# Optimization experiments

Measured on AMD Instinct MI355X. Metric: run time of the kernel, lower is better.

## Reference

```python
import jax, jax.numpy as jnp
import numpy as np
from jax import lax

# ---- config constants (mirror init_kwargs) ----
PC_MIN_X, PC_MIN_Y, PC_MIN_Z = 0.0, -40.0, -3.0
PC_MAX_X, PC_MAX_Y, PC_MAX_Z = 70.4, 40.0, 1.0
VX, VY = 0.05, 0.05
NUM_KEYPOINTS = 2048
RADII = (0.4, 0.8)
NSAMPLE = (16, 16)
EPS = 1e-5


def setup_inputs() -> dict:
    key = jax.random.key(0)
    ks = jax.random.split(key, 16)
    B, N = 2, 32768
    u = jax.random.uniform(ks[0], (B, N, 4), dtype=jnp.float32)
    x = u[..., 0] * (PC_MAX_X - PC_MIN_X) + PC_MIN_X
    y = u[..., 1] * (PC_MAX_Y - PC_MIN_Y) + PC_MIN_Y
    z = u[..., 2] * (PC_MAX_Z - PC_MIN_Z) + PC_MIN_Z
    points = jnp.stack([x, y, z, u[..., 3]], axis=-1)  # (B,N,4): xyz + intensity
    spatial_features = jax.random.normal(ks[1], (B, 256, 200, 176), dtype=jnp.float32)
    p = lambda k, s: jax.random.normal(k, s, dtype=jnp.float32) * 0.1
    return dict(
        points=points, spatial_features=spatial_features,
        w0_0=p(ks[2], (4, 16)), g0_0=jnp.ones(16), b0_0=jnp.zeros(16),
        w0_1=p(ks[3], (16, 16)), g0_1=jnp.ones(16), b0_1=jnp.zeros(16),
        w1_0=p(ks[4], (4, 16)), g1_0=jnp.ones(16), b1_0=jnp.zeros(16),
        w1_1=p(ks[5], (16, 16)), g1_1=jnp.ones(16), b1_1=jnp.zeros(16),
        wf=p(ks[6], (288, 128)), gf=jnp.ones(128), bf=jnp.zeros(128),
        bev_stride=8,
    )


def _bn(x, g, b, axes):
    m = jnp.mean(x, axis=axes, keepdims=True)
    v = jnp.var(x, axis=axes, keepdims=True)
    return (x - m) * lax.rsqrt(v + EPS) * g + b


def _fps(xyz, K):
    # farthest point sampling, pointnet2 semantics (start at index 0)
    B, N, _ = xyz.shape
    def step(carry, _):
        dists, last = carry
        p = jax.vmap(lambda a, i: a[i])(xyz, last)           # (B,3)
        d = jnp.sum((xyz - p[:, None, :]) ** 2, axis=-1)     # (B,N)
        dists = jnp.minimum(dists, d)
        nxt = jnp.argmax(dists, axis=-1).astype(jnp.int32)
        return (dists, nxt), nxt
    init = (jnp.full((B, N), 1e10, xyz.dtype), jnp.zeros((B,), jnp.int32))
    _, rest = lax.scan(step, init, None, length=K - 1)       # (K-1,B)
    return jnp.concatenate([jnp.zeros((B, 1), jnp.int32), rest.T], axis=1)  # (B,K)


def _ball_group_pool(pts, kp, dist2, radius, ns, layers):
    # pts: (B,N,4) xyz+feat, kp: (B,K,3), dist2: (B,K,N) (stop-grad)
    B, N = pts.shape[0], pts.shape[1]
    valid = dist2 < radius * radius
    score = jnp.where(valid, -jnp.arange(N, dtype=jnp.float32), -jnp.inf)
    vals, idx = lax.top_k(score, ns)                          # first ns in-radius indices
    ok = jnp.isfinite(vals)                                   # (B,K,ns)
    idx = jnp.where(ok, idx, idx[..., :1])                    # duplicate first valid
    empty = ~ok[..., 0]                                       # (B,K) no neighbor at all
    grouped = jax.vmap(lambda p, i: p[i])(pts, idx)           # (B,K,ns,4)
    rel = grouped[..., :3] - kp[:, :, None, :]
    h = jnp.concatenate([rel, grouped[..., 3:]], axis=-1)     # (B,K,ns,4)
    h = jnp.where(empty[..., None, None], 0.0, h)
    for w, g, b in layers:
        h = jax.nn.relu(_bn(h @ w, g, b, axes=(0, 1, 2)))
    pooled = jnp.max(h, axis=2)                               # (B,K,C)
    return jnp.where(empty[..., None], 0.0, pooled)


def _bev_interp(kp, bev, stride):
    # kp: (B,K,3), bev: (B,C,H,W); torch bilinear_interpolate semantics
    B, C, H, W = bev.shape
    xi = (kp[..., 0] - PC_MIN_X) / VX / stride                # (B,K)
    yi = (kp[..., 1] - PC_MIN_Y) / VY / stride
    x0 = jnp.clip(jnp.floor(xi).astype(jnp.int32), 0, W - 1)
    x1 = jnp.clip(jnp.floor(xi).astype(jnp.int32) + 1, 0, W - 1)
    y0 = jnp.clip(jnp.floor(yi).astype(jnp.int32), 0, H - 1)
    y1 = jnp.clip(jnp.floor(yi).astype(jnp.int32) + 1, 0, H - 1)
    gat = jax.vmap(lambda f, yy, xx: f[:, yy, xx].T)          # (K,C) per batch
    Ia, Ib = gat(bev, y0, x0), gat(bev, y1, x0)
    Ic, Id = gat(bev, y0, x1), gat(bev, y1, x1)
    x0f, x1f = x0.astype(jnp.float32), x1.astype(jnp.float32)
    y0f, y1f = y0.astype(jnp.float32), y1.astype(jnp.float32)
    wa = ((x1f - xi) * (y1f - yi))[..., None]
    wb = ((x1f - xi) * (yi - y0f))[..., None]
    wc = ((xi - x0f) * (y1f - yi))[..., None]
    wd = ((xi - x0f) * (yi - y0f))[..., None]
    return Ia * wa + Ib * wb + Ic * wc + Id * wd              # (B,K,C)


def reference(points, spatial_features, w0_0, g0_0, b0_0, w0_1, g0_1, b0_1,
              w1_0, g1_0, b1_0, w1_1, g1_1, b1_1, wf, gf, bf, bev_stride):
    xyz = points[..., :3]                                     # (B,N,3)
    idx = _fps(xyz, NUM_KEYPOINTS)                            # (B,K)
    kp = jax.vmap(lambda p, i: p[i])(xyz, idx)                # keypoints (B,K,3)

    # BEV bilinear interpolation
    bev_feats = _bev_interp(kp, spatial_features, bev_stride) # (B,K,256)

    # raw-points multi-scale ball-query aggregation
    dist2 = lax.stop_gradient(
        jnp.sum((kp[:, :, None, :] - xyz[:, None, :, :]) ** 2, axis=-1))  # (B,K,N)
    p0 = _ball_group_pool(points, kp, dist2, RADII[0], NSAMPLE[0],
                          [(w0_0, g0_0, b0_0), (w0_1, g0_1, b0_1)])
    p1 = _ball_group_pool(points, kp, dist2, RADII[1], NSAMPLE[1],
                          [(w1_0, g1_0, b1_0), (w1_1, g1_1, b1_1)])

    feat = jnp.concatenate([bev_feats, p0, p1], axis=-1)      # (B,K,288)
    M = feat.shape[0] * feat.shape[1]
    feat = feat.reshape(M, -1)
    h = feat @ wf                                             # Linear no bias
    h = _bn(h, gf, bf, axes=(0,))                             # BatchNorm1d (train mode)
    return jax.nn.relu(h)                                     # (M,128)
```

## Files before the change

kernel.cpp:

```cpp
#include <hip/hip_runtime.h>
#include <hip/hip_bf16.h>
#include <limits.h>
#include <cstddef>

#define B_SZ    2
#define N_PTS   32768
#define N_KP    2048
#define N_CHUNK 512
#define H_BEV   200
#define W_BEV   176
#define C_BEV   256
#define FEAT_DIM 288
#define C_OUT   128
#define M_ROWS  4096

__device__ __forceinline__ float sqd(float ax, float ay, float az,
                                     float bx, float by, float bz) {
  float dx = ax - bx, dy = ay - by, dz = az - bz;
  return __fadd_rn(__fadd_rn(dx * dx, dy * dy), dz * dz);
}

__device__ __forceinline__ unsigned part1by1(unsigned n) {
  n &= 0xFFFF;
  n = (n | (n << 8)) & 0x00FF00FF;
  n = (n | (n << 4)) & 0x0F0F0F0F;
  n = (n | (n << 2)) & 0x33333333;
  n = (n | (n << 1)) & 0x55555555;
  return n;
}

#define DPP_MOV(v, CTRL, RMASK) \
  ((unsigned)__builtin_amdgcn_update_dpp((int)(v), (int)(v), (CTRL), (RMASK), 0xf, false))

__device__ __forceinline__ unsigned wave_umax_bcast(unsigned v) {
  unsigned t;
  t = DPP_MOV(v, 0x111, 0xf); v = v > t ? v : t;
  t = DPP_MOV(v, 0x112, 0xf); v = v > t ? v : t;
  t = DPP_MOV(v, 0x114, 0xf); v = v > t ? v : t;
  t = DPP_MOV(v, 0x118, 0xf); v = v > t ? v : t;
  t = DPP_MOV(v, 0x142, 0xa); v = v > t ? v : t;
  t = DPP_MOV(v, 0x143, 0xc); v = v > t ? v : t;
  return (unsigned)__builtin_amdgcn_readlane((int)v, 63);
}
__device__ __forceinline__ unsigned wave_umin_bcast(unsigned v) {
  unsigned t;
  t = DPP_MOV(v, 0x111, 0xf); v = v < t ? v : t;
  t = DPP_MOV(v, 0x112, 0xf); v = v < t ? v : t;
  t = DPP_MOV(v, 0x114, 0xf); v = v < t ? v : t;
  t = DPP_MOV(v, 0x118, 0xf); v = v < t ? v : t;
  t = DPP_MOV(v, 0x142, 0xa); v = v < t ? v : t;
  t = DPP_MOV(v, 0x143, 0xc); v = v < t ? v : t;
  return (unsigned)__builtin_amdgcn_readlane((int)v, 63);
}

#define R64_STEP(hi, lo, CTRL, RMASK)                                         \
  {                                                                           \
    unsigned hm_ = DPP_MOV(hi, CTRL, RMASK);                                  \
    unsigned lm_ = DPP_MOV(lo, CTRL, RMASK);                                  \
    bool gt_ = (hm_ > (hi)) || (hm_ == (hi) && lm_ > (lo));                   \
    hi = gt_ ? hm_ : (hi); lo = gt_ ? lm_ : (lo);                             \
  }

#define R64_ALL(hi, lo)                                                       \
  R64_STEP(hi, lo, 0x111, 0xf)                                                \
  R64_STEP(hi, lo, 0x112, 0xf)                                                \
  R64_STEP(hi, lo, 0x114, 0xf)                                                \
  R64_STEP(hi, lo, 0x118, 0xf)                                                \
  R64_STEP(hi, lo, 0x142, 0xa)                                                \
  R64_STEP(hi, lo, 0x143, 0xc)

__global__ void cell_count(const float4* __restrict__ pts,
                           int* __restrict__ codes, int* __restrict__ counts) {
  const int b = blockIdx.x, tid = threadIdx.x;
  __shared__ int cnt[4096];
  for (int k = tid; k < 4096; k += 1024) cnt[k] = 0;
  __syncthreads();
  for (int j = 0; j < 32; ++j) {
    int i = j * 1024 + tid;
    float4 v = pts[(size_t)b * N_PTS + i];
    int cx = min(63, max(0, (int)(v.x * (64.0f / 70.4f))));
    int cy = min(63, max(0, (int)((v.y + 40.0f) * 0.8f)));
    int code = (int)(part1by1((unsigned)cx) | (part1by1((unsigned)cy) << 1));
    codes[(size_t)b * N_PTS + i] = code;
    atomicAdd(&cnt[code], 1);
  }
  __syncthreads();
  for (int k = tid; k < 4096; k += 1024) counts[b * 4096 + k] = cnt[k];
}

__global__ void cell_scan(const int* __restrict__ counts, int* __restrict__ offs) {
  const int b = blockIdx.x, lane = threadIdx.x;
  const int* cnt = counts + b * 4096;
  int* off = offs + b * 4096;
  int s = 0;
  for (int k = 0; k < 64; ++k) s += cnt[lane * 64 + k];
  int incl = s;
#pragma unroll
  for (int o = 1; o < 64; o <<= 1) {
    int t = __shfl_up(incl, o);
    if (lane >= o) incl += t;
  }
  int run = incl - s;
  for (int k = 0; k < 64; ++k) {
    int id = lane * 64 + k;
    int t = cnt[id];
    off[id] = run;
    run += t;
  }
}

__global__ void scatter_pts(const float4* __restrict__ pts,
                            const int* __restrict__ codes,
                            int* __restrict__ offs,
                            float4* __restrict__ spts, int* __restrict__ sorig) {
  const int b = blockIdx.x, tid = threadIdx.x;
  for (int j = 0; j < 32; ++j) {
    int i = j * 1024 + tid;
    int code = codes[(size_t)b * N_PTS + i];
    int pos = atomicAdd(&offs[b * 4096 + code], 1);
    spts[(size_t)b * N_PTS + pos] = pts[(size_t)b * N_PTS + i];
    sorig[(size_t)b * N_PTS + pos] = i;
  }
}

__global__ void chunk_bbox(const float4* __restrict__ spts, float* __restrict__ bbox) {
  const int wid = threadIdx.x >> 6, lane = threadIdx.x & 63;
  const int chunk = blockIdx.x * 4 + wid;
  const int b = chunk >> 9, c = chunk & (N_CHUNK - 1);
  float4 v = spts[(size_t)b * N_PTS + c * 64 + lane];
  float lx = v.x, ly = v.y, lz = v.z, hx = v.x, hy = v.y, hz = v.z;
#pragma unroll
  for (int o = 32; o >= 1; o >>= 1) {
    lx = fminf(lx, __shfl_xor(lx, o)); hx = fmaxf(hx, __shfl_xor(hx, o));
    ly = fminf(ly, __shfl_xor(ly, o)); hy = fmaxf(hy, __shfl_xor(hy, o));
    lz = fminf(lz, __shfl_xor(lz, o)); hz = fmaxf(hz, __shfl_xor(hz, o));
  }
  if (lane == 0) {
    float* bp = bbox + (size_t)chunk * 6;
    bp[0] = lx; bp[1] = ly; bp[2] = lz; bp[3] = hx; bp[4] = hy; bp[5] = hz;
  }
}

__global__ void fps_pruned(const float4* __restrict__ pts,
                           const float4* __restrict__ spts,
                           const int* __restrict__ sorig,
                           const float* __restrict__ bbox,
                           float4* __restrict__ kp_xyz) {
  const int b = blockIdx.x;
  const int tid = threadIdx.x;
  const int wid = tid >> 6, lane = tid & 63;
  const float4* p4o = pts + (size_t)b * N_PTS;
  const float4* sp4 = spts + (size_t)b * N_PTS;
  const int* sog = sorig + (size_t)b * N_PTS;
  const unsigned long long below = (lane == 0) ? 0ull : ((~0ull) >> (64 - lane));

  __shared__ float d_lds[N_PTS];
  __shared__ float keyd[N_CHUNK];
  __shared__ int keyo[N_CHUNK];
  __shared__ float keyx[N_CHUNK];
  __shared__ float keyy[N_CHUNK];
  __shared__ float keyz[N_CHUNK];
  __shared__ int dirty_s[2][N_CHUNK];
  __shared__ int ndirty_s[2];

  for (int i = tid; i < N_PTS; i += 1024) d_lds[i] = 1e10f;
  if (tid < N_CHUNK) keyd[tid] = 1e10f;
  if (tid < 2) ndirty_s[tid] = 0;
  float bx0 = 0.f, by0 = 0.f, bz0 = 0.f, bx1 = 0.f, by1 = 0.f, bz1 = 0.f;
  if (tid < N_CHUNK) {
    const float* bp = bbox + (size_t)b * N_CHUNK * 6 + (size_t)tid * 6;
    bx0 = bp[0]; by0 = bp[1]; bz0 = bp[2]; bx1 = bp[3]; by1 = bp[4]; bz1 = bp[5];
  }
  float4 p0 = p4o[0];
  float sx = p0.x, sy = p0.y, sz = p0.z;
  if (tid == 0) kp_xyz[b * N_KP] = make_float4(sx, sy, sz, 0.f);
  __syncthreads();

#define PROC_CHUNK(cc, pp, og, dp)                                            \
  {                                                                           \
    float ss = sqd((pp).x, (pp).y, (pp).z, sx, sy, sz);                       \
    float nd = fminf((dp), ss);                                               \
    d_lds[((cc) << 6) + lane] = nd;                                           \
    unsigned nb = __float_as_uint(nd);          \
    unsigned mb = wave_umax_bcast(nb);                                        \
    unsigned cnd = (nb == mb) ? (unsigned)(og) : 0xFFFFFFFFu;                 \
    cnd = wave_umin_bcast(cnd);                                               \
    if ((unsigned)(og) == cnd) {                                              \
      keyd[cc] = __uint_as_float(mb); keyo[cc] = (int)cnd;                    \
      keyx[cc] = (pp).x; keyy[cc] = (pp).y; keyz[cc] = (pp).z;                \
    }                                                                         \
  }

  for (int it = 1; it < N_KP; ++it) {
    const int s = it & 1;
    bool dirty = false;
    if (tid < N_CHUNK) {
      float dxm = fmaxf(fmaxf(bx0 - sx, sx - bx1), 0.f);
      float dym = fmaxf(fmaxf(by0 - sy, sy - by1), 0.f);
      float dzm = fmaxf(fmaxf(bz0 - sz, sz - bz1), 0.f);
      float lb = (dxm * dxm + dym * dym) + dzm * dzm;
      dirty = lb * 0.99999f < keyd[tid];
    }
    unsigned long long m = __ballot(dirty);
    if (tid < N_CHUNK) {
      int cw = (int)__popcll(m);
      int base = 0;
      if (lane == 0 && cw) base = atomicAdd(&ndirty_s[s], cw);
      base = __builtin_amdgcn_readfirstlane(base);
      if (dirty) dirty_s[s][base + (int)__popcll(m & below)] = tid;
    }
    if (tid == 1023) ndirty_s[s ^ 1] = 0;
    __syncthreads();
    const int K = ndirty_s[s];
    {
      int cA = (wid < K) ? dirty_s[s][wid] : -1;
      int cB = ((wid + 16) < K) ? dirty_s[s][wid + 16] : -1;
      if (cA >= 0) {
        int iA = (cA << 6) + lane;
        float4 pA = sp4[iA];
        int ogA = sog[iA];
        float dpA = d_lds[iA];
        if (cB >= 0) {
          int iB = (cB << 6) + lane;
          float4 pB = sp4[iB];
          int ogB = sog[iB];
          float dpB = d_lds[iB];
          PROC_CHUNK(cA, pA, ogA, dpA);
          PROC_CHUNK(cB, pB, ogB, dpB);
        } else {
          PROC_CHUNK(cA, pA, ogA, dpA);
        }
        for (int r = 2; r * 16 < K; ++r) {
          int ci = r * 16 + wid;
          if (ci < K) {
            int c = dirty_s[s][ci];
            int i2 = (c << 6) + lane;
            float4 p = sp4[i2];
            int og2 = sog[i2];
            float dp2 = d_lds[i2];
            PROC_CHUNK(c, p, og2, dp2);
          }
        }
      }
    }
    __syncthreads();
    {
      unsigned hi = __float_as_uint(keyd[lane]);
      unsigned lo = 0xFFFFFFFFu - (unsigned)keyo[lane];
      unsigned ch = (unsigned)lane;
#pragma unroll
      for (int j = 1; j < 8; ++j) {
        int c = j * 64 + lane;
        unsigned h2 = __float_as_uint(keyd[c]);
        unsigned l2 = 0xFFFFFFFFu - (unsigned)keyo[c];
        bool gt = (h2 > hi) || (h2 == hi && l2 > lo);
        hi = gt ? h2 : hi; lo = gt ? l2 : lo; ch = gt ? (unsigned)c : ch;
      }
      unsigned hl = hi, ll = lo;
      R64_ALL(hi, lo)
      unsigned mb = (unsigned)__builtin_amdgcn_readlane((int)hi, 63);
      unsigned cn = (unsigned)__builtin_amdgcn_readlane((int)lo, 63);
      unsigned long long cm = __ballot(hl == mb && ll == cn);
      int cl = (int)__builtin_ctzll(cm);
      int cb = (int)(unsigned)__builtin_amdgcn_readlane((int)ch, cl);
      sx = keyx[cb]; sy = keyy[cb]; sz = keyz[cb];
      if (tid == 0) kp_xyz[b * N_KP + it] = make_float4(sx, sy, sz, 0.f);
    }
  }
#undef PROC_CHUNK
}

__global__ void bev_kernel(const float4* __restrict__ kp,
                           const float* __restrict__ bev,
                           const int* __restrict__ stride_p,
                           float* __restrict__ feat) {
  const int kpi = blockIdx.x;
  const int c = threadIdx.x;
  const int b = kpi >> 11;
  float4 k = kp[kpi];
  float sf = (float)stride_p[0];
  float xi = (k.x - 0.0f) / 0.05f / sf;
  float yi = (k.y - (-40.0f)) / 0.05f / sf;
  int fx = (int)floorf(xi), fy = (int)floorf(yi);
  int x0 = min(max(fx, 0), W_BEV - 1), x1 = min(max(fx + 1, 0), W_BEV - 1);
  int y0 = min(max(fy, 0), H_BEV - 1), y1 = min(max(fy + 1, 0), H_BEV - 1);
  float x0f = (float)x0, x1f = (float)x1, y0f = (float)y0, y1f = (float)y1;
  float wa = (x1f - xi) * (y1f - yi);
  float wb = (x1f - xi) * (yi - y0f);
  float wc = (xi - x0f) * (y1f - yi);
  float wd = (xi - x0f) * (yi - y0f);
  const float* fb = bev + (size_t)b * C_BEV * (H_BEV * W_BEV) + (size_t)c * (H_BEV * W_BEV);
  float Ia = fb[y0 * W_BEV + x0], Ib = fb[y1 * W_BEV + x0];
  float Ic = fb[y0 * W_BEV + x1], Id = fb[y1 * W_BEV + x1];
  feat[(size_t)kpi * FEAT_DIM + c] = ((Ia * wa + Ib * wb) + Ic * wc) + Id * wd;
}

__device__ __forceinline__ int sel4(int q, int a, int b, int c, int d) {
  return q == 0 ? a : (q == 1 ? b : (q == 2 ? c : d));
}

__global__ void ballq_kernel(const float4* __restrict__ pts,
                             const float4* __restrict__ kp,
                             int* __restrict__ lists,
                             int* __restrict__ cnts) {
  const int w = threadIdx.x >> 6;
  const int lane = threadIdx.x & 63;
  const int kpbase = blockIdx.x * 16 + w * 4;
  const int b = blockIdx.x >> 7;
  const float4* p4 = pts + (size_t)b * N_PTS;
  __shared__ int l0[4][4][16];
  __shared__ int l1[4][4][16];
  float kx[4], ky[4], kz[4];
  int c0[4] = {0, 0, 0, 0}, c1[4] = {0, 0, 0, 0};
#pragma unroll
  for (int q = 0; q < 4; ++q) {
    float4 kq = kp[kpbase + q];
    kx[q] = kq.x; ky[q] = kq.y; kz[q] = kq.z;
  }
  const float R0SQ = (float)(0.4 * 0.4);
  const float R1SQ = (float)(0.8 * 0.8);
  const unsigned long long below = (lane == 0) ? 0ull : ((~0ull) >> (64 - lane));

  for (int r = 0; r < N_PTS / 64; ++r) {
    const int i = r * 64 + lane;
    float4 v = p4[i];
#pragma unroll
    for (int q = 0; q < 4; ++q) {
      float dd = sqd(v.x, v.y, v.z, kx[q], ky[q], kz[q]);
      bool in1 = dd < R1SQ;
      unsigned long long m1 = __ballot(in1);
      if (m1) {
        bool in0 = dd < R0SQ;
        unsigned long long m0 = __ballot(in0);
        if (c0[q] < 16) {
          if (in0) { int pos = c0[q] + __popcll(m0 & below); if (pos < 16) l0[w][q][pos] = i; }
          c0[q] += __popcll(m0);
        }
        if (c1[q] < 16) {
          if (in1) { int pos = c1[q] + __popcll(m1 & below); if (pos < 16) l1[w][q][pos] = i; }
          c1[q] += __popcll(m1);
        }
      }
    }
  }
  int q = lane >> 4, s = lane & 15;
  int kpi = kpbase + q;
  int cA = sel4(q, min(c0[0], 16), min(c0[1], 16), min(c0[2], 16), min(c0[3], 16));
  int cB = sel4(q, min(c1[0], 16), min(c1[1], 16), min(c1[2], 16), min(c1[3], 16));
  int vA = (s < cA) ? l0[w][q][s] : (cA > 0 ? l0[w][q][0] : 0);
  int vB = (s < cB) ? l1[w][q][s] : (cB > 0 ? l1[w][q][0] : 0);
  lists[(size_t)(0 * M_ROWS + kpi) * 16 + s] = vA;
  lists[(size_t)(1 * M_ROWS + kpi) * 16 + s] = vB;
  if (lane < 4) {
    cnts[0 * M_ROWS + kpbase + lane] = sel4(lane, min(c0[0], 16), min(c0[1], 16), min(c0[2], 16), min(c0[3], 16));
    cnts[1 * M_ROWS + kpbase + lane] = sel4(lane, min(c1[0], 16), min(c1[1], 16), min(c1[2], 16), min(c1[3], 16));
  }
}

__global__ void group_mlp1(const float4* __restrict__ pts,
                           const float4* __restrict__ kp,
                           const int* __restrict__ lists,
                           const int* __restrict__ cnts,
                           const float* __restrict__ w00,
                           const float* __restrict__ w10,
                           float* __restrict__ abuf) {
  int gid = blockIdx.x * 256 + threadIdx.x;
  int br = gid >> 16;
  int rem = gid & 65535;
  int bkp = rem >> 4, s = rem & 15;
  int b = bkp >> 11;
  __shared__ float wl[64];
  if (threadIdx.x < 64) wl[threadIdx.x] = (br ? w10 : w00)[threadIdx.x];
  __syncthreads();
  int cnt = cnts[br * M_ROWS + bkp];
  float h0 = 0.f, h1 = 0.f, h2 = 0.f, h3 = 0.f;
  if (cnt > 0) {
    int pidx = lists[(size_t)(br * M_ROWS + bkp) * 16 + s];
    float4 p = pts[(size_t)b * N_PTS + pidx];
    float4 k = kp[bkp];
    h0 = p.x - k.x; h1 = p.y - k.y; h2 = p.z - k.z; h3 = p.w;
  }
  float* out = abuf + (size_t)gid * 16;
#pragma unroll
  for (int c = 0; c < 16; ++c)
    out[c] = ((h0 * wl[c] + h1 * wl[16 + c]) + h2 * wl[32 + c]) + h3 * wl[48 + c];
}

__global__ void stats16_partial(const float* __restrict__ a, float* __restrict__ part) {
  int br = blockIdx.y, bl = blockIdx.x, t = threadIdx.x;
  const float* base = a + (size_t)br * 65536 * 16;
  float s[16], q[16];
#pragma unroll
  for (int c = 0; c < 16; ++c) { s[c] = 0.f; q[c] = 0.f; }
  for (int rr = 0; rr < 4; ++rr) {
    int row = bl * 1024 + rr * 256 + t;
#pragma unroll
    for (int c = 0; c < 16; ++c) {
      float v = base[(size_t)row * 16 + c];
      s[c] += v; q[c] += v * v;
    }
  }
  __shared__ float sbs[256][16];
  __shared__ float sbq[256][16];
#pragma unroll
  for (int c = 0; c < 16; ++c) { sbs[t][c] = s[c]; sbq[t][c] = q[c]; }
  __syncthreads();
  for (int st = 128; st > 0; st >>= 1) {
    if (t < st) {
#pragma unroll
      for (int c = 0; c < 16; ++c) { sbs[t][c] += sbs[t + st][c]; sbq[t][c] += sbq[t + st][c]; }
    }
    __syncthreads();
  }
  if (t < 16) {
    part[(size_t)(br * 64 + bl) * 32 + t] = sbs[0][t];
    part[(size_t)(br * 64 + bl) * 32 + 16 + t] = sbq[0][t];
  }
}

__global__ void stats16_final(const float* __restrict__ part, float* __restrict__ stats) {
  int t = threadIdx.x;
  if (t < 32) {
    int br = t >> 4, c = t & 15;
    float s = 0.f, q = 0.f;
    for (int bl = 0; bl < 64; ++bl) {
      s += part[(size_t)(br * 64 + bl) * 32 + c];
      q += part[(size_t)(br * 64 + bl) * 32 + 16 + c];
    }
    float m = s / 65536.f;
    float var = q / 65536.f - m * m;
    stats[(br * 16 + c) * 2] = m;
    stats[(br * 16 + c) * 2 + 1] = rsqrtf(var + 1e-5f);
  }
}

__global__ void mlp2_kernel(float* __restrict__ abuf, const float* __restrict__ stats,
                            const float* __restrict__ g00, const float* __restrict__ b00,
                            const float* __restrict__ g10, const float* __restrict__ b10,
                            const float* __restrict__ w01, const float* __restrict__ w11) {
  int gid = blockIdx.x * 256 + threadIdx.x;
  int br = gid >> 16;
  __shared__ float wl[256];
  wl[threadIdx.x] = (br ? w11 : w01)[threadIdx.x];
  __syncthreads();
  const float* g = br ? g10 : g00;
  const float* bb = br ? b10 : b00;
  float* row = abuf + (size_t)gid * 16;
  float z[16];
#pragma unroll
  for (int f = 0; f < 16; ++f) {
    float m = stats[(br * 16 + f) * 2], is = stats[(br * 16 + f) * 2 + 1];
    z[f] = fmaxf(0.f, (row[f] - m) * is * g[f] + bb[f]);
  }
  float o[16];
#pragma unroll
  for (int c = 0; c < 16; ++c) o[c] = 0.f;
#pragma unroll
  for (int f = 0; f < 16; ++f) {
#pragma unroll
    for (int c = 0; c < 16; ++c) o[c] += z[f] * wl[f * 16 + c];
  }
#pragma unroll
  for (int c = 0; c < 16; ++c) row[c] = o[c];
}

__global__ void pool_kernel(const float* __restrict__ abuf, const float* __restrict__ stats,
                            const int* __restrict__ cnts,
                            const float* __restrict__ g01, const float* __restrict__ b01,
                            const float* __restrict__ g11, const float* __restrict__ b11,
                            float* __restrict__ feat) {
  int gid = blockIdx.x * 256 + threadIdx.x;
  int br = gid >> 16;
  int rem = gid & 65535;
  int bkp = rem >> 4, c = rem & 15;
  const float* g = br ? g11 : g01;
  const float* bb = br ? b11 : b01;
  float m = stats[(br * 16 + c) * 2], is = stats[(br * 16 + c) * 2 + 1];
  float gg = g[c], bv = bb[c];
  const float* base = abuf + ((size_t)br * 65536 + (size_t)bkp * 16) * 16 + c;
  float mx = -1e30f;
#pragma unroll
  for (int s = 0; s < 16; ++s) {
    float v = base[(size_t)s * 16];
    mx = fmaxf(mx, fmaxf(0.f, (v - m) * is * gg + bv));
  }
  if (cnts[br * M_ROWS + bkp] == 0) mx = 0.f;
  feat[(size_t)bkp * FEAT_DIM + 256 + br * 16 + c] = mx;
}

__global__ void final_mm(const float* __restrict__ feat, const float* __restrict__ wf,
                         float* __restrict__ hbuf) {
  int row = blockIdx.x;
  int c = threadIdx.x;
  __shared__ float fr[FEAT_DIM];
  for (int k = c; k < FEAT_DIM; k += 128) fr[k] = feat[(size_t)row * FEAT_DIM + k];
  __syncthreads();
  float acc = 0.f;
#pragma unroll 8
  for (int k = 0; k < FEAT_DIM; ++k) acc += fr[k] * wf[(size_t)k * C_OUT + c];
  hbuf[(size_t)row * C_OUT + c] = acc;
}

__global__ void stats128_partial(const float* __restrict__ hbuf, float* __restrict__ part) {
  int bl = blockIdx.x, c = threadIdx.x;
  float s = 0.f, q = 0.f;
  for (int r = 0; r < 128; ++r) {
    float v = hbuf[(size_t)(bl * 128 + r) * C_OUT + c];
    s += v; q += v * v;
  }
  part[(size_t)(bl * 128 + c) * 2] = s;
  part[(size_t)(bl * 128 + c) * 2 + 1] = q;
}

__global__ void stats128_final(const float* __restrict__ part, float* __restrict__ stats) {
  int c = threadIdx.x;
  float s = 0.f, q = 0.f;
  for (int bl = 0; bl < 32; ++bl) {
    s += part[(size_t)(bl * 128 + c) * 2];
    q += part[(size_t)(bl * 128 + c) * 2 + 1];
  }
  float m = s / 4096.f;
  float var = q / 4096.f - m * m;
  stats[c * 2] = m;
  stats[c * 2 + 1] = rsqrtf(var + 1e-5f);
}

__global__ void out_kernel(const float* __restrict__ hbuf, const float* __restrict__ stats,
                           const float* __restrict__ gf, const float* __restrict__ bf,
                           float* __restrict__ out) {
  int gid = blockIdx.x * 256 + threadIdx.x;
  int c = gid & 127;
  float v = hbuf[gid];
  float r = fmaxf(0.f, (v - stats[c * 2]) * stats[c * 2 + 1] * gf[c] + bf[c]);
  out[gid] = r;
}

extern "C" void kernel_launch(void* const* d_in, const int* in_sizes, int n_in,
                              void* d_out, int out_size, void* d_ws, size_t ws_size,
                              hipStream_t stream) {
  const float4* pts = (const float4*)d_in[0];
  const float* spatial = (const float*)d_in[1];
  const float* w0_0 = (const float*)d_in[2];
  const float* g0_0 = (const float*)d_in[3];
  const float* b0_0 = (const float*)d_in[4];
  const float* w0_1 = (const float*)d_in[5];
  const float* g0_1 = (const float*)d_in[6];
  const float* b0_1 = (const float*)d_in[7];
  const float* w1_0 = (const float*)d_in[8];
  const float* g1_0 = (const float*)d_in[9];
  const float* b1_0 = (const float*)d_in[10];
  const float* w1_1 = (const float*)d_in[11];
  const float* g1_1 = (const float*)d_in[12];
  const float* b1_1 = (const float*)d_in[13];
  const float* wf  = (const float*)d_in[14];
  const float* gf  = (const float*)d_in[15];
  const float* bfp = (const float*)d_in[16];
  const int* stride_p = (const int*)d_in[17];

  char* ws = (char*)d_ws;
  float4* kp_xyz = (float4*)(ws + 0);
  int* lists     = (int*)(ws + 65536);
  int* cnts      = (int*)(ws + 589824);
  float* abuf    = (float*)(ws + 622592);
  float* feat    = (float*)(ws + 9011200);
  float* hbuf    = (float*)(ws + 13729792);
  float* part16  = (float*)(ws + 15826944);
  float* stats16 = (float*)(ws + 15843328);
  float* part128 = (float*)(ws + 15843584);
  float* stats128= (float*)(ws + 15876352);

  char* sbase = (char*)abuf;
  float4* spts = (float4*)(sbase + 0);
  int* sorig   = (int*)(sbase + 1048576);
  int* codes   = (int*)(sbase + 1310720);
  int* counts  = (int*)(sbase + 1572864);
  int* offs    = (int*)(sbase + 1605632);
  float* bboxg = (float*)(sbase + 1638400);

  cell_count<<<B_SZ, 1024, 0, stream>>>(pts, codes, counts);
  cell_scan<<<B_SZ, 64, 0, stream>>>(counts, offs);
  scatter_pts<<<B_SZ, 1024, 0, stream>>>(pts, codes, offs, spts, sorig);
  chunk_bbox<<<256, 256, 0, stream>>>(spts, bboxg);
  fps_pruned<<<B_SZ, 1024, 0, stream>>>(pts, spts, sorig, bboxg, kp_xyz);
  bev_kernel<<<M_ROWS, 256, 0, stream>>>(kp_xyz, spatial, stride_p, feat);
  ballq_kernel<<<256, 256, 0, stream>>>(pts, kp_xyz, lists, cnts);
  group_mlp1<<<512, 256, 0, stream>>>(pts, kp_xyz, lists, cnts, w0_0, w1_0, abuf);
  stats16_partial<<<dim3(64, 2), 256, 0, stream>>>(abuf, part16);
  stats16_final<<<1, 64, 0, stream>>>(part16, stats16);
  mlp2_kernel<<<512, 256, 0, stream>>>(abuf, stats16, g0_0, b0_0, g1_0, b1_0, w0_1, w1_1);
  stats16_partial<<<dim3(64, 2), 256, 0, stream>>>(abuf, part16);
  stats16_final<<<1, 64, 0, stream>>>(part16, stats16);
  pool_kernel<<<512, 256, 0, stream>>>(abuf, stats16, cnts, g0_1, b0_1, g1_1, b1_1, feat);
  final_mm<<<M_ROWS, 128, 0, stream>>>(feat, wf, hbuf);
  stats128_partial<<<32, 128, 0, stream>>>(hbuf, part128);
  stats128_final<<<1, 128, 0, stream>>>(part128, stats128);
  out_kernel<<<2048, 256, 0, stream>>>(hbuf, stats128, gf, bfp, (float*)d_out);
}
```

Measured before the change: 3.732 ms.

## Restructure FPS: per-wave chunk ownership, packed index, sorted chunks, ballot argmax

The point's original index is packed into the w field of the sorted points, and each 64-point chunk is bitonic-sorted by that index. Within a chunk the first maximal lane is then the lowest original index, so one ballot plus ctz replaces the second wave min-reduction. The FPS kernel drops to 512 threads and gives each wave a fixed set of chunks, with bounding boxes and chunk keys held in registers. This removes the shared dirty-list compaction, its atomics and one barrier per iteration, but adds a barrier at the end of each iteration and a little per-wave load imbalance.

```diff
diff --git a/kernel.cpp b/kernel.cpp
--- a/kernel.cpp
+++ b/kernel.cpp
@@ -42,16 +42,6 @@
   t = DPP_MOV(v, 0x143, 0xc); v = v > t ? v : t;
   return (unsigned)__builtin_amdgcn_readlane((int)v, 63);
 }
-__device__ __forceinline__ unsigned wave_umin_bcast(unsigned v) {
-  unsigned t;
-  t = DPP_MOV(v, 0x111, 0xf); v = v < t ? v : t;
-  t = DPP_MOV(v, 0x112, 0xf); v = v < t ? v : t;
-  t = DPP_MOV(v, 0x114, 0xf); v = v < t ? v : t;
-  t = DPP_MOV(v, 0x118, 0xf); v = v < t ? v : t;
-  t = DPP_MOV(v, 0x142, 0xa); v = v < t ? v : t;
-  t = DPP_MOV(v, 0x143, 0xc); v = v < t ? v : t;
-  return (unsigned)__builtin_amdgcn_readlane((int)v, 63);
-}
 
 #define R64_STEP(hi, lo, CTRL, RMASK)                                         \
   {                                                                           \
@@ -112,15 +102,42 @@
 __global__ void scatter_pts(const float4* __restrict__ pts,
                             const int* __restrict__ codes,
                             int* __restrict__ offs,
-                            float4* __restrict__ spts, int* __restrict__ sorig) {
+                            float4* __restrict__ spts) {
   const int b = blockIdx.x, tid = threadIdx.x;
   for (int j = 0; j < 32; ++j) {
     int i = j * 1024 + tid;
     int code = codes[(size_t)b * N_PTS + i];
     int pos = atomicAdd(&offs[b * 4096 + code], 1);
-    spts[(size_t)b * N_PTS + pos] = pts[(size_t)b * N_PTS + i];
-    sorig[(size_t)b * N_PTS + pos] = i;
-  }
+    float4 v = pts[(size_t)b * N_PTS + i];
+    v.w = __int_as_float(i);
+    spts[(size_t)b * N_PTS + pos] = v;
+  }
+}
+
+__global__ void chunk_sort(float4* __restrict__ spts) {
+  const int wid = threadIdx.x >> 6, lane = threadIdx.x & 63;
+  const int chunk = blockIdx.x * 4 + wid;
+  const int b = chunk >> 9, c = chunk & (N_CHUNK - 1);
+  float4 v = spts[(size_t)b * N_PTS + c * 64 + lane];
+  float x = v.x, y = v.y, z = v.z, w = v.w;
+  int key = __float_as_int(w);
+#pragma unroll
+  for (int k = 2; k <= 64; k <<= 1) {
+#pragma unroll
+    for (int j = k >> 1; j > 0; j >>= 1) {
+      float xx = __shfl_xor(x, j);
+      float yy = __shfl_xor(y, j);
+      float zz = __shfl_xor(z, j);
+      float ww = __shfl_xor(w, j);
+      int kk = __float_as_int(ww);
+      bool lower = (lane & j) == 0;
+      bool up = (lane & k) == 0;
+      bool cmp = key > kk;
+      bool takeOther = cmp ^ lower ^ up;
+      if (takeOther) { x = xx; y = yy; z = zz; w = ww; key = kk; }
+    }
+  }
+  spts[(size_t)b * N_PTS + c * 64 + lane] = make_float4(x, y, z, w);
 }
 
 __global__ void chunk_bbox(const float4* __restrict__ spts, float* __restrict__ bbox) {
@@ -143,7 +160,6 @@
 
 __global__ void fps_pruned(const float4* __restrict__ pts,
                            const float4* __restrict__ spts,
-                           const int* __restrict__ sorig,
                            const float* __restrict__ bbox,
                            float4* __restrict__ kp_xyz) {
   const int b = blockIdx.x;
@@ -151,8 +167,6 @@
   const int wid = tid >> 6, lane = tid & 63;
   const float4* p4o = pts + (size_t)b * N_PTS;
   const float4* sp4 = spts + (size_t)b * N_PTS;
-  const int* sog = sorig + (size_t)b * N_PTS;
-  const unsigned long long below = (lane == 0) ? 0ull : ((~0ull) >> (64 - lane));
 
   __shared__ float d_lds[N_PTS];
   __shared__ float keyd[N_CHUNK];
@@ -160,87 +174,69 @@
   __shared__ float keyx[N_CHUNK];
   __shared__ float keyy[N_CHUNK];
   __shared__ float keyz[N_CHUNK];
-  __shared__ int dirty_s[2][N_CHUNK];
-  __shared__ int ndirty_s[2];
-
-  for (int i = tid; i < N_PTS; i += 1024) d_lds[i] = 1e10f;
-  if (tid < N_CHUNK) keyd[tid] = 1e10f;
-  if (tid < 2) ndirty_s[tid] = 0;
-  float bx0 = 0.f, by0 = 0.f, bz0 = 0.f, bx1 = 0.f, by1 = 0.f, bz1 = 0.f;
-  if (tid < N_CHUNK) {
-    const float* bp = bbox + (size_t)b * N_CHUNK * 6 + (size_t)tid * 6;
-    bx0 = bp[0]; by0 = bp[1]; bz0 = bp[2]; bx1 = bp[3]; by1 = bp[4]; bz1 = bp[5];
-  }
+
+  for (int i = tid; i < N_PTS; i += 512) d_lds[i] = 1e10f;
+  if (tid < N_CHUNK) { keyd[tid] = 1e10f; keyo[tid] = 0; keyx[tid] = 0.f; keyy[tid] = 0.f; keyz[tid] = 0.f; }
+
+  const int cown = lane * 8 + wid;
+  const float* bp = bbox + (size_t)b * N_CHUNK * 6 + (size_t)cown * 6;
+  float bx0 = bp[0], by0 = bp[1], bz0 = bp[2];
+  float bx1 = bp[3], by1 = bp[4], bz1 = bp[5];
+  float kreg = 1e10f;
+
   float4 p0 = p4o[0];
   float sx = p0.x, sy = p0.y, sz = p0.z;
   if (tid == 0) kp_xyz[b * N_KP] = make_float4(sx, sy, sz, 0.f);
   __syncthreads();
 
-#define PROC_CHUNK(cc, pp, og, dp)                                            \
+#define PROC_CHUNK(cc, pp, dp)                                                \
   {                                                                           \
     float ss = sqd((pp).x, (pp).y, (pp).z, sx, sy, sz);                       \
     float nd = fminf((dp), ss);                                               \
     d_lds[((cc) << 6) + lane] = nd;                                           \
     unsigned nb = __float_as_uint(nd);          \
     unsigned mb = wave_umax_bcast(nb);                                        \
-    unsigned cnd = (nb == mb) ? (unsigned)(og) : 0xFFFFFFFFu;                 \
-    cnd = wave_umin_bcast(cnd);                                               \
-    if ((unsigned)(og) == cnd) {                                              \
-      keyd[cc] = __uint_as_float(mb); keyo[cc] = (int)cnd;                    \
+    unsigned long long win = __ballot(nb == mb);                              \
+    int cl = (int)__builtin_ctzll(win);          \
+    if (lane == ((cc) >> 3)) kreg = __uint_as_float(mb);                      \
+    if (lane == cl) {                                                         \
+      keyd[cc] = __uint_as_float(mb);                                         \
+      keyo[cc] = __float_as_int((pp).w);                                      \
       keyx[cc] = (pp).x; keyy[cc] = (pp).y; keyz[cc] = (pp).z;                \
     }                                                                         \
   }
 
   for (int it = 1; it < N_KP; ++it) {
-    const int s = it & 1;
-    bool dirty = false;
-    if (tid < N_CHUNK) {
-      float dxm = fmaxf(fmaxf(bx0 - sx, sx - bx1), 0.f);
-      float dym = fmaxf(fmaxf(by0 - sy, sy - by1), 0.f);
-      float dzm = fmaxf(fmaxf(bz0 - sz, sz - bz1), 0.f);
-      float lb = (dxm * dxm + dym * dym) + dzm * dzm;
-      dirty = lb * 0.99999f < keyd[tid];
-    }
-    unsigned long long m = __ballot(dirty);
-    if (tid < N_CHUNK) {
-      int cw = (int)__popcll(m);
-      int base = 0;
-      if (lane == 0 && cw) base = atomicAdd(&ndirty_s[s], cw);
-      base = __builtin_amdgcn_readfirstlane(base);
-      if (dirty) dirty_s[s][base + (int)__popcll(m & below)] = tid;
-    }
-    if (tid == 1023) ndirty_s[s ^ 1] = 0;
-    __syncthreads();
-    const int K = ndirty_s[s];
+    float dxm = fmaxf(fmaxf(bx0 - sx, sx - bx1), 0.f);
+    float dym = fmaxf(fmaxf(by0 - sy, sy - by1), 0.f);
+    float dzm = fmaxf(fmaxf(bz0 - sz, sz - bz1), 0.f);
+    float lb = (dxm * dxm + dym * dym) + dzm * dzm;
+    bool dirty = lb * 0.99999f < kreg;
+    unsigned long long mask = __ballot(dirty);
     {
-      int cA = (wid < K) ? dirty_s[s][wid] : -1;
-      int cB = ((wid + 16) < K) ? dirty_s[s][wid + 16] : -1;
-      if (cA >= 0) {
-        int iA = (cA << 6) + lane;
-        float4 pA = sp4[iA];
-        int ogA = sog[iA];
-        float dpA = d_lds[iA];
-        if (cB >= 0) {
-          int iB = (cB << 6) + lane;
-          float4 pB = sp4[iB];
-          int ogB = sog[iB];
-          float dpB = d_lds[iB];
-          PROC_CHUNK(cA, pA, ogA, dpA);
-          PROC_CHUNK(cB, pB, ogB, dpB);
-        } else {
-          PROC_CHUNK(cA, pA, ogA, dpA);
-        }
-        for (int r = 2; r * 16 < K; ++r) {
-          int ci = r * 16 + wid;
-          if (ci < K) {
-            int c = dirty_s[s][ci];
-            int i2 = (c << 6) + lane;
-            float4 p = sp4[i2];
-            int og2 = sog[i2];
-            float dp2 = d_lds[i2];
-            PROC_CHUNK(c, p, og2, dp2);
-          }
-        }
+      int cA = 0, cB = 0; bool hasA = false, hasB = false;
+      float4 pA, pB; float dpA = 0.f, dpB = 0.f;
+      if (mask) {
+        int l = (int)__builtin_ctzll(mask); mask &= mask - 1; hasA = true;
+        cA = l * 8 + wid;
+        int i = (cA << 6) + lane;
+        pA = sp4[i]; dpA = d_lds[i];
+      }
+      if (mask) {
+        int l = (int)__builtin_ctzll(mask); mask &= mask - 1; hasB = true;
+        cB = l * 8 + wid;
+        int i = (cB << 6) + lane;
+        pB = sp4[i]; dpB = d_lds[i];
+      }
+      while (hasA) {
+        PROC_CHUNK(cA, pA, dpA);
+        cA = cB; pA = pB; dpA = dpB; hasA = hasB;
+        if (mask) {
+          int l = (int)__builtin_ctzll(mask); mask &= mask - 1; hasB = true;
+          cB = l * 8 + wid;
+          int i = (cB << 6) + lane;
+          pB = sp4[i]; dpB = d_lds[i];
+        } else hasB = false;
       }
     }
     __syncthreads();
@@ -266,6 +262,7 @@
       sx = keyx[cb]; sy = keyy[cb]; sz = keyz[cb];
       if (tid == 0) kp_xyz[b * N_KP + it] = make_float4(sx, sy, sz, 0.f);
     }
+    __syncthreads();
   }
 #undef PROC_CHUNK
 }
@@ -571,17 +568,17 @@
 
   char* sbase = (char*)abuf;
   float4* spts = (float4*)(sbase + 0);
-  int* sorig   = (int*)(sbase + 1048576);
-  int* codes   = (int*)(sbase + 1310720);
-  int* counts  = (int*)(sbase + 1572864);
-  int* offs    = (int*)(sbase + 1605632);
-  float* bboxg = (float*)(sbase + 1638400);
+  int* codes   = (int*)(sbase + 1048576);
+  int* counts  = (int*)(sbase + 1310720);
+  int* offs    = (int*)(sbase + 1343488);
+  float* bboxg = (float*)(sbase + 1376256);
 
   cell_count<<<B_SZ, 1024, 0, stream>>>(pts, codes, counts);
   cell_scan<<<B_SZ, 64, 0, stream>>>(counts, offs);
-  scatter_pts<<<B_SZ, 1024, 0, stream>>>(pts, codes, offs, spts, sorig);
+  scatter_pts<<<B_SZ, 1024, 0, stream>>>(pts, codes, offs, spts);
+  chunk_sort<<<256, 256, 0, stream>>>(spts);
   chunk_bbox<<<256, 256, 0, stream>>>(spts, bboxg);
-  fps_pruned<<<B_SZ, 1024, 0, stream>>>(pts, spts, sorig, bboxg, kp_xyz);
+  fps_pruned<<<B_SZ, 512, 0, stream>>>(pts, spts, bboxg, kp_xyz);
   bev_kernel<<<M_ROWS, 256, 0, stream>>>(kp_xyz, spatial, stride_p, feat);
   ballq_kernel<<<256, 256, 0, stream>>>(pts, kp_xyz, lists, cnts);
   group_mlp1<<<512, 256, 0, stream>>>(pts, kp_xyz, lists, cnts, w0_0, w1_0, abuf);
```

After: 3.334 ms (median of 2 runs). -10.7%, faster.
